# Performance work log

Measured on AMD Instinct MI355X. Metric: run time of the kernel, lower is better.

## Reference

```python
import jax, jax.numpy as jnp
import numpy as np

B, S, E = 32, 128, 128
NQ, NS = 100000, 512
QN, SN = 4, 10
S_MAX = 4
NEG = -1e30


def setup_inputs() -> dict:
    key = jax.random.key(0)
    ks = jax.random.split(key, 24)
    def nrm(k, shape, sc):
        return jax.random.normal(k, shape, jnp.float32) * sc
    inp = {}
    inp['question'] = jax.random.randint(ks[0], (B, S), 0, NQ, jnp.int32)
    inp['response'] = jax.random.randint(ks[1], (B, S), 0, 2, jnp.int32)
    inp['mask'] = jax.random.randint(ks[2], (B, S), 0, 2, jnp.int32)
    inp['q_neighbors'] = jax.random.randint(ks[3], (NQ, QN), 0, NS, jnp.int32)
    inp['s_neighbors'] = jax.random.randint(ks[4], (NS, SN), 0, NQ, jnp.int32)
    sidx = jax.random.randint(ks[5], (NQ, S_MAX), 0, NS, jnp.int32)
    inp['qs_table'] = jnp.zeros((NQ, NS), jnp.float32).at[jnp.arange(NQ)[:, None], sidx].set(1.0)
    inp['emb_q'] = nrm(ks[6], (NQ, E), 1.0)
    inp['emb_s'] = nrm(ks[7], (NS, E), 1.0)
    inp['emb_r'] = nrm(ks[8], (2, E), 1.0)
    s_in = 1.0 / np.sqrt(2 * E).astype(np.float32)
    s_e = 1.0 / np.sqrt(E).astype(np.float32)
    inp['W_ih'] = nrm(ks[9], (4 * E, 2 * E), s_in)
    inp['b_ih'] = nrm(ks[10], (4 * E,), s_in)
    inp['b_hh'] = nrm(ks[11], (4 * E,), s_in)
    inp['W_agg'] = nrm(ks[12], (3, E, E), s_e)
    inp['b_agg'] = nrm(ks[13], (3, E), s_e)
    inp['W_last'] = nrm(ks[14], (E, E), s_e)
    inp['b_last'] = nrm(ks[15], (E,), s_e)
    inp['W_query'] = nrm(ks[16], (E, E), s_e)
    inp['b_query'] = nrm(ks[17], (E,), s_e)
    inp['W_key'] = nrm(ks[18], (E, E), s_e)
    inp['b_key'] = nrm(ks[19], (E,), s_e)
    inp['w_W'] = nrm(ks[20], (2 * E,), s_in)
    inp['b_W'] = nrm(ks[21], (), s_in)
    return inp


def _forward(question, response, mask, q_neighbors, s_neighbors, qs_table,
             emb_q, emb_s, emb_r, W_ih, b_ih, b_hh, W_agg, b_agg, W_last, b_last,
             W_query, b_query, W_key, b_key, w_W, b_W):
    Bq, Sq = question.shape
    Ed = emb_q.shape[1]
    AGG = W_agg.shape[0]
    w_q, w_k = w_W[:Ed], w_W[Ed:]
    c_pad = jnp.tanh(b_query) @ w_k  # attention logit piece of an all-zero padded state
    pos = jnp.arange(Sq)

    def step(state_history, xs):
        t, q_t, r_t, m_t, q_next = xs
        # ---- multi-hop neighbor gather (q -> s -> q -> s) ----
        n1 = q_neighbors[q_t]              # [B,QN] skill ids
        n2 = s_neighbors[n1]               # [B,QN,SN] question ids
        n3 = q_neighbors[n2]               # [B,QN,SN,QN] skill ids
        e = [emb_q[q_t], emb_s[n1], emb_q[n2], emb_s[n3]]
        # triangular mean-aggregate (dropout is identity in eval mode)
        for i in range(AGG):
            for j in range(AGG - i):
                e[j] = jnp.tanh((e[j + 1].mean(-2) + e[j]) @ W_agg[j].T + b_agg[j])
        agg = jnp.tanh(e[0] @ W_last.T + b_last)
        emb_qt = jnp.where((m_t == 1)[:, None], agg, emb_q[q_t])
        # ---- LSTMCell with zero initial (h, c): W_hh @ 0 drops out, b_hh remains ----
        x = jnp.concatenate([emb_qt, emb_r[r_t]], -1)
        gates = x @ W_ih.T + b_ih + b_hh
        gi, gf, gg, go = jnp.split(gates, 4, -1)
        h = jax.nn.sigmoid(go) * jnp.tanh(jax.nn.sigmoid(gi) * jnp.tanh(gg))
        # ---- skills related to next question; zero-padded rows contribute exactly 0 ----
        vals, sidx = jax.lax.top_k(qs_table[q_next], S_MAX)
        emb_sk = emb_s[sidx] * (vals > 0.0)[..., None]
        qs_concat = jnp.concatenate([emb_q[q_next][:, None], emb_sk], 1)  # [B,1+S_MAX,E]
        # ---- hard recap: history steps whose question is a 2-hop neighbor of q_next ----
        q_rel = s_neighbors[q_neighbors[q_next]].reshape(Bq, -1)          # [B,QN*SN]
        matches = (question[:, :, None] == q_rel[:, None, :]).any(-1) & (pos[None, :] < t)
        n_sel = matches.sum(-1)
        P = (jnp.max(n_sel) - n_sel).astype(jnp.float32)  # zero-pad count to per-batch max
        # ---- predict: MLP_W(concat(Q,K)) is rank-1 => logit = a[b,q] + c[b,s] ----
        a = jnp.tanh(qs_concat @ W_key.T + b_key) @ w_q + b_W             # [B,Qd]
        c_hist = jnp.tanh(state_history @ W_query.T + b_query) @ w_k      # [B,S]
        c_cur = jnp.tanh(h @ W_query.T + b_query) @ w_k                   # [B]
        lh = jnp.where(matches[:, None, :], a[:, :, None] + c_hist[:, None, :], NEG)
        lc = a + c_cur[:, None]
        lp = a + c_pad
        m = jnp.maximum(jnp.maximum(lh.max(-1), lc), lp)
        Eh = jnp.exp(lh - m[:, :, None])
        Ec = jnp.exp(lc - m)
        Ep = jnp.exp(lp - m)
        g_hist = jnp.einsum('bqe,bse->bqs', qs_concat, state_history)
        g_cur = jnp.einsum('bqe,be->bq', qs_concat, h)
        denom = Eh.sum(-1) + Ec + P[:, None] * Ep  # zero-pad states counted analytically
        num = (Eh * g_hist).sum(-1) + Ec * g_cur   # pads multiply g=0 -> no numerator term
        y = jax.nn.sigmoid(jnp.sum(num / denom, axis=1))
        # original skips the state write at t == 0 (slot 0 stays zero forever)
        state_history = state_history.at[:, t].set(jnp.where(t > 0, h, jnp.zeros_like(h)))
        return state_history, y

    ts = jnp.arange(Sq - 1)
    xs = (ts, question[:, :-1].T, response[:, :-1].T, mask[:, :-1].T, question[:, 1:].T)
    init = jnp.zeros((Bq, Sq, Ed), jnp.float32)
    _, ys = jax.lax.scan(step, init, xs)
    return jnp.zeros((Bq, Sq), jnp.float32).at[:, 0].set(0.5).at[:, 1:].set(ys.T)


def reference(question, response, mask, q_neighbors, s_neighbors, qs_table,
              emb_q, emb_s, emb_r, W_ih, b_ih, b_hh, W_agg, b_agg, W_last, b_last,
              W_query, b_query, W_key, b_key, w_W, b_W):
    return _forward(question, response, mask, q_neighbors, s_neighbors, qs_table,
                    emb_q, emb_s, emb_r, W_ih, b_ih, b_hh, W_agg, b_agg, W_last, b_last,
                    W_query, b_query, W_key, b_key, w_W, b_W)
```

## Files before the change

kernel.cpp:

```cpp
#include <hip/hip_runtime.h>
#include <stdint.h>

#define NB 32
#define SEQ 128
#define EMB 128
#define NSTEP 127
#define NS 512

__device__ __forceinline__ float ftanh(float x){ float e=__expf(2.f*x); return 1.f-2.f/(e+1.f); }
__device__ __forceinline__ float fsig(float x){ return 1.f/(1.f+__expf(-x)); }
__device__ __forceinline__ float4 ld4(const float* p){ return *(const float4*)p; }

#define FMA_COL(acc, xv) \
  acc.x = fmaf(xv.x, w0.x, fmaf(xv.y, w1.x, fmaf(xv.z, w2.x, fmaf(xv.w, w3.x, acc.x)))); \
  acc.y = fmaf(xv.x, w0.y, fmaf(xv.y, w1.y, fmaf(xv.z, w2.y, fmaf(xv.w, w3.y, acc.y)))); \
  acc.z = fmaf(xv.x, w0.z, fmaf(xv.y, w1.z, fmaf(xv.z, w2.z, fmaf(xv.w, w3.z, acc.z)))); \
  acc.w = fmaf(xv.x, w0.w, fmaf(xv.y, w1.w, fmaf(xv.z, w2.w, fmaf(xv.w, w3.w, acc.w))));

template<int K, int XS>
__device__ __forceinline__ void gemm16(const float* __restrict__ WT, int NEtot,
                                       const float* __restrict__ Xl,
                                       const float* __restrict__ bias,
                                       float* __restrict__ outb )
{
  const int tid = threadIdx.x;
  const int et = tid & 31;
  const int rt = tid >> 5;
  const float* wp = WT + et*4;
  const float* x0 = Xl + (rt*2)*XS;
  const float* x1 = x0 + XS;
  float4 acc0 = {0.f,0.f,0.f,0.f}, acc1 = {0.f,0.f,0.f,0.f};
  float4 w0 = ld4(wp);
  float4 w1 = ld4(wp + NEtot);
  float4 w2 = ld4(wp + 2*NEtot);
  float4 w3 = ld4(wp + 3*NEtot);
  float4 xa = ld4(x0), xb = ld4(x1);
  #pragma unroll 8
  for (int k = 4; k < K; k += 4) {
    const float* wn = wp + (size_t)k*NEtot;
    float4 m0 = ld4(wn);
    float4 m1 = ld4(wn + NEtot);
    float4 m2 = ld4(wn + 2*NEtot);
    float4 m3 = ld4(wn + 3*NEtot);
    float4 ya = ld4(x0 + k), yb = ld4(x1 + k);
    FMA_COL(acc0, xa); FMA_COL(acc1, xb);
    w0=m0; w1=m1; w2=m2; w3=m3; xa=ya; xb=yb;
  }
  FMA_COL(acc0, xa); FMA_COL(acc1, xb);
  float4 bb = ld4(bias + et*4);
  acc0.x+=bb.x; acc0.y+=bb.y; acc0.z+=bb.z; acc0.w+=bb.w;
  acc1.x+=bb.x; acc1.y+=bb.y; acc1.z+=bb.z; acc1.w+=bb.w;
  *(float4*)(outb + (rt*2)*132 + et*4) = acc0;
  *(float4*)(outb + (rt*2+1)*132 + et*4) = acc1;
}
#undef FMA_COL

__global__ __launch_bounds__(256) void k_T(
    const float* __restrict__ W_agg, const float* __restrict__ W_last,
    const float* __restrict__ W_query, const float* __restrict__ W_ih,
    const float* __restrict__ b_ih, const float* __restrict__ b_hh,
    const float* __restrict__ b_query, const float* __restrict__ w_W,
    float* __restrict__ WT012, float* __restrict__ WLT, float* __restrict__ WQT,
    float* __restrict__ WIHT, float* __restrict__ BIH, float* __restrict__ CPAD)
{
  const int gid = blockIdx.x*256 + threadIdx.x;
  const int gsz = gridDim.x*256;
  for (int i = gid; i < 49152; i += gsz) {
    int j = i >> 14, rem = i & 16383, k = rem >> 7, e = rem & 127;
    WT012[i] = W_agg[j*16384 + e*128 + k];
  }
  for (int i = gid; i < 16384; i += gsz) {
    int k = i >> 7, e = i & 127;
    WLT[i] = W_last[e*128 + k];
    WQT[i] = W_query[e*128 + k];
  }
  for (int i = gid; i < 131072; i += gsz) {
    int k = i >> 9, e = i & 511;
    WIHT[i] = W_ih[e*256 + k];
  }
  for (int i = gid; i < 512; i += gsz) BIH[i] = b_ih[i] + b_hh[i];
  if (blockIdx.x == 0) {
    __shared__ float red[256];
    float v = (threadIdx.x < 128) ? ftanh(b_query[threadIdx.x]) * w_W[128 + threadIdx.x] : 0.f;
    red[threadIdx.x] = v; __syncthreads();
    #pragma unroll
    for (int s = 128; s > 0; s >>= 1) {
      if (threadIdx.x < s) red[threadIdx.x] += red[threadIdx.x + s];
      __syncthreads();
    }
    if (threadIdx.x == 0) CPAD[0] = red[0];
  }
}

__global__ __launch_bounds__(256) void k_pre(
    const int* __restrict__ s_neighbors, const int* __restrict__ q_neighbors,
    const float* __restrict__ emb_q, const float* __restrict__ emb_s,
    const float* __restrict__ WT012, const float* __restrict__ b_agg,
    float* __restrict__ E1, float* __restrict__ G1)
{
  __shared__ float XA[16*132];
  __shared__ float XB[16*132];
  __shared__ int idx[160];
  __shared__ int n3[64];
  const int tid = threadIdx.x;
  const int blk = blockIdx.x;
  if (blk < 32) {
    const int s0 = blk*16;
    if (tid < 160) idx[tid] = s_neighbors[s0*10 + tid];
    __syncthreads();
    for (int f = tid; f < 512; f += 256) {
      int r = f >> 5, e4 = (f & 31) << 2;
      float4 a = ld4(emb_s + (size_t)(s0+r)*128 + e4);
      float sx=0,sy=0,sz=0,sw=0;
      #pragma unroll
      for (int jj = 0; jj < 10; ++jj) {
        float4 q = ld4(emb_q + (size_t)idx[r*10+jj]*128 + e4);
        sx+=q.x; sy+=q.y; sz+=q.z; sw+=q.w;
      }
      float4 o; o.x=a.x+0.1f*sx; o.y=a.y+0.1f*sy; o.z=a.z+0.1f*sz; o.w=a.w+0.1f*sw;
      *(float4*)(XA + r*132 + e4) = o;
    }
    __syncthreads();
    gemm16<128,132>(WT012 + 16384, 128, XA, b_agg + 128, XB);
    __syncthreads();
    for (int f = tid; f < 2048; f += 256) {
      int r = f >> 7, e = f & 127;
      E1[(size_t)(s0+r)*128 + e] = ftanh(XB[r*132 + e]);
    }
  } else {
    const int p0 = (blk-32)*16;
    if (tid < 16) idx[tid] = s_neighbors[p0 + tid];
    __syncthreads();
    if (tid < 64) n3[tid] = q_neighbors[(size_t)idx[tid>>2]*4 + (tid&3)];
    __syncthreads();
    for (int f = tid; f < 512; f += 256) {
      int r = f >> 5, e4 = (f & 31) << 2;
      float4 a = ld4(emb_q + (size_t)idx[r]*128 + e4);
      float sx=0,sy=0,sz=0,sw=0;
      #pragma unroll
      for (int k = 0; k < 4; ++k) {
        float4 q = ld4(emb_s + (size_t)n3[r*4+k]*128 + e4);
        sx+=q.x; sy+=q.y; sz+=q.z; sw+=q.w;
      }
      float4 o; o.x=a.x+0.25f*sx; o.y=a.y+0.25f*sy; o.z=a.z+0.25f*sz; o.w=a.w+0.25f*sw;
      *(float4*)(XA + r*132 + e4) = o;
    }
    __syncthreads();
    gemm16<128,132>(WT012 + 32768, 128, XA, b_agg + 256, XB);
    __syncthreads();
    for (int f = tid; f < 2048; f += 256) {
      int r = f >> 7, e = f & 127;
      atomicAdd(&G1[(size_t)((p0+r)/10)*128 + e], ftanh(XB[r*132 + e]));
    }
  }
}

__global__ __launch_bounds__(256) void k_pre2(
    const float* __restrict__ E1, const float* __restrict__ G1,
    const float* __restrict__ WT012, const float* __restrict__ b_agg,
    float* __restrict__ E2)
{
  __shared__ float XA[16*132];
  __shared__ float XB[16*132];
  const int tid = threadIdx.x;
  const int s0 = blockIdx.x*16;
  for (int f = tid; f < 2048; f += 256) {
    int r = f >> 7, e = f & 127;
    XA[r*132 + e] = 0.1f*G1[(size_t)(s0+r)*128 + e] + E1[(size_t)(s0+r)*128 + e];
  }
  __syncthreads();
  gemm16<128,132>(WT012 + 16384, 128, XA, b_agg + 128, XB);
  __syncthreads();
  for (int f = tid; f < 2048; f += 256) {
    int r = f >> 7, e = f & 127;
    E2[(size_t)(s0+r)*128 + e] = ftanh(XB[r*132 + e]);
  }
}

__global__ __launch_bounds__(256) void k_chain(
    const int* __restrict__ question, const int* __restrict__ response,
    const int* __restrict__ maskp, const int* __restrict__ q_neighbors,
    const float* __restrict__ emb_q, const float* __restrict__ emb_s,
    const float* __restrict__ emb_r,
    const float* __restrict__ WT012, const float* __restrict__ WLT,
    const float* __restrict__ WQT, const float* __restrict__ WIHT,
    const float* __restrict__ BIH,
    const float* __restrict__ b_agg, const float* __restrict__ b_last,
    const float* __restrict__ b_query, const float* __restrict__ w_W,
    const float* __restrict__ E1, const float* __restrict__ E2,
    float* __restrict__ Hfull, float* __restrict__ Cq)
{
  __shared__ float P_[12688];
  __shared__ int qts[16], rts[16], mts[16], n1s[64];
  float* XA = P_;
  float* XB = P_ + 2112;
  float* M1 = P_ + 4224;
  float* M2 = P_ + 6272;
  float* G3 = P_ + 4224;
  float* XC = P_ + 8448;
  float* cq = P_ + 12672;

  const int tid = threadIdx.x;
  const int blk = blockIdx.x;

  if (tid < 16) {
    int rid = blk*16 + tid;
    int b = rid / 127, t = rid - b*127;
    qts[tid] = question[b*SEQ + t];
    rts[tid] = response[b*SEQ + t];
    mts[tid] = maskp[b*SEQ + t];
    cq[tid] = 0.f;
  }
  __syncthreads();
  if (tid < 64) n1s[tid] = q_neighbors[(size_t)qts[tid>>2]*4 + (tid&3)];
  __syncthreads();
  for (int f = tid; f < 512; f += 256) {
    int r = f >> 5, e4 = (f & 31) << 2;
    const int* nn = n1s + r*4;
    float4 a = ld4(emb_q + (size_t)qts[r]*128 + e4);
    float s1x=0,s1y=0,s1z=0,s1w=0, s2x=0,s2y=0,s2z=0,s2w=0, s3x=0,s3y=0,s3z=0,s3w=0;
    #pragma unroll
    for (int i = 0; i < 4; ++i) {
      float4 q1 = ld4(emb_s + (size_t)nn[i]*128 + e4);
      float4 q2 = ld4(E1 + (size_t)nn[i]*128 + e4);
      float4 q3 = ld4(E2 + (size_t)nn[i]*128 + e4);
      s1x+=q1.x; s1y+=q1.y; s1z+=q1.z; s1w+=q1.w;
      s2x+=q2.x; s2y+=q2.y; s2z+=q2.z; s2w+=q2.w;
      s3x+=q3.x; s3y+=q3.y; s3z+=q3.z; s3w+=q3.w;
    }
    float4 o; o.x=a.x+0.25f*s1x; o.y=a.y+0.25f*s1y; o.z=a.z+0.25f*s1z; o.w=a.w+0.25f*s1w;
    *(float4*)(XA + r*132 + e4) = o;
    float4 p; p.x=0.25f*s2x; p.y=0.25f*s2y; p.z=0.25f*s2z; p.w=0.25f*s2w;
    *(float4*)(M1 + r*128 + e4) = p;
    float4 u; u.x=0.25f*s3x; u.y=0.25f*s3y; u.z=0.25f*s3z; u.w=0.25f*s3w;
    *(float4*)(M2 + r*128 + e4) = u;
  }
  __syncthreads();
  gemm16<128,132>(WT012, 128, XA, b_agg, XB);
  __syncthreads();
  for (int f = tid; f < 2048; f += 256) {
    int r = f >> 7, e = f & 127;
    XB[r*132 + e] = M1[r*128 + e] + ftanh(XB[r*132 + e]);
  }
  __syncthreads();
  gemm16<128,132>(WT012, 128, XB, b_agg, XA);
  __syncthreads();
  for (int f = tid; f < 2048; f += 256) {
    int r = f >> 7, e = f & 127;
    XA[r*132 + e] = M2[r*128 + e] + ftanh(XA[r*132 + e]);
  }
  __syncthreads();
  gemm16<128,132>(WT012, 128, XA, b_agg, XB);
  __syncthreads();
  for (int f = tid; f < 2048; f += 256) {
    int r = f >> 7, e = f & 127;
    XB[r*132 + e] = ftanh(XB[r*132 + e]);
  }
  __syncthreads();
  gemm16<128,132>(WLT, 128, XB, b_last, XA);
  __syncthreads();
  for (int f = tid; f < 2048; f += 256) {
    int r = f >> 7, e = f & 127;
    float agg = ftanh(XA[r*132 + e]);
    XC[r*264 + e] = (mts[r] == 1) ? agg : emb_q[(size_t)qts[r]*128 + e];
    XC[r*264 + 128 + e] = emb_r[rts[r]*128 + e];
  }
  __syncthreads();
  gemm16<256,264>(WIHT,       512, XC, BIH,       XA);
  gemm16<256,264>(WIHT + 256, 512, XC, BIH + 256, XB);
  gemm16<256,264>(WIHT + 384, 512, XC, BIH + 384, G3);
  __syncthreads();
  for (int f = tid; f < 2048; f += 256) {
    int r = f >> 7, e = f & 127;
    float gi = XA[r*132 + e], gg = XB[r*132 + e], go = G3[r*132 + e];
    float h = fsig(go) * ftanh(fsig(gi) * ftanh(gg));
    XC[r*264 + e] = h;
    Hfull[(size_t)(blk*16 + r)*128 + e] = h;
  }
  __syncthreads();
  gemm16<128,264>(WQT, 128, XC, b_query, XA);
  __syncthreads();
  {
    const int et = tid & 31, rt = tid >> 5;
    const float* wk = w_W + 128 + et*4;
    float4 wv = ld4(wk);
    #pragma unroll
    for (int rr = 0; rr < 2; ++rr) {
      int r = rt*2 + rr;
      const float* o = XA + r*132 + et*4;
      float s = ftanh(o[0])*wv.x + ftanh(o[1])*wv.y + ftanh(o[2])*wv.z + ftanh(o[3])*wv.w;
      atomicAdd(&cq[r], s);
    }
  }
  __syncthreads();
  if (tid < 16) Cq[blk*16 + tid] = cq[tid];
}

__global__ __launch_bounds__(128) void k_match_t(
    const int* __restrict__ question, const int* __restrict__ q_neighbors,
    const int* __restrict__ s_neighbors,
    int* __restrict__ nsel, unsigned long long* __restrict__ mwords,
    float* __restrict__ Pmax)
{
  __shared__ int nq[4];
  __shared__ int qr[40];
  __shared__ unsigned long long wv[2];
  const int tid = threadIdx.x;
  const int t = blockIdx.x;
  int pm = 0;
  for (int b = 0; b < NB; ++b) {
    const int q_next = question[b*SEQ + t + 1];
    if (tid < 4) nq[tid] = q_neighbors[(size_t)q_next*4 + tid];
    __syncthreads();
    if (tid < 40) qr[tid] = s_neighbors[(size_t)nq[tid/10]*10 + tid%10];
    __syncthreads();
    bool pred = false;
    if (tid < t) {
      int qp = question[b*SEQ + tid];
      #pragma unroll 8
      for (int i = 0; i < 40; ++i) pred |= (qp == qr[i]);
    }
    unsigned long long bal = __ballot(pred);
    if ((tid & 63) == 0) wv[tid >> 6] = bal;
    __syncthreads();
    if (tid == 0) {
      mwords[((size_t)b*NSTEP + t)*2 + 0] = wv[0];
      mwords[((size_t)b*NSTEP + t)*2 + 1] = wv[1];
      int ns = __popcll(wv[0]) + __popcll(wv[1]);
      nsel[b*NSTEP + t] = ns;
      pm = max(pm, ns);
    }
    __syncthreads();
  }
  if (tid == 0) Pmax[t] = (float)pm;
}

__device__ __forceinline__ float bsum128(float v, float* red) {
  const int tid = threadIdx.x;
  __syncthreads();
  red[tid] = v;
  __syncthreads();
  #pragma unroll
  for (int s = 64; s > 0; s >>= 1) {
    if (tid < s) red[tid] += red[tid + s];
    __syncthreads();
  }
  return red[0];
}
__device__ __forceinline__ float bmax128(float v, float* red) {
  const int tid = threadIdx.x;
  __syncthreads();
  red[tid] = v;
  __syncthreads();
  #pragma unroll
  for (int s = 64; s > 0; s >>= 1) {
    if (tid < s) red[tid] = fmaxf(red[tid], red[tid + s]);
    __syncthreads();
  }
  return red[0];
}

__global__ __launch_bounds__(128) void k_attn(
    const int* __restrict__ question, const float* __restrict__ qs_table,
    const float* __restrict__ emb_q, const float* __restrict__ emb_s,
    const float* __restrict__ CPAD,
    const float* __restrict__ Hfull, const float* __restrict__ Cq,
    const int* __restrict__ nsel, const unsigned long long* __restrict__ mwords,
    const float* __restrict__ Pmax, float* __restrict__ out)
{
  __shared__ float red[128];
  __shared__ float us[128];
  __shared__ int cols[8];
  __shared__ int cnt;
  const int tid = threadIdx.x;
  const int bid = blockIdx.x;
  const int b = bid / NSTEP, t = bid % NSTEP;
  const size_t bt = (size_t)b*NSTEP + t;
  const int q_next = question[b*SEQ + t + 1];

  if (tid == 0) cnt = 0;
  __syncthreads();
  #pragma unroll
  for (int m = 0; m < 4; ++m) {
    int c = tid + 128*m;
    float v = qs_table[(size_t)q_next*NS + c];
    if (v > 0.f) {
      int p = atomicAdd(&cnt, 1);
      if (p < 8) cols[p] = c;
    }
  }
  __syncthreads();
  const int nc = min(cnt, 4);
  {
    float ue = emb_q[(size_t)q_next*EMB + tid];
    for (int i = 0; i < nc; ++i) ue += emb_s[(size_t)cols[i]*EMB + tid];
    us[tid] = ue;
  }
  const float c_pad = CPAD[0];
  const float P = Pmax[t] - (float)nsel[bt];

  const unsigned long long w0 = mwords[bt*2 + 0];
  const unsigned long long w1 = mwords[bt*2 + 1];
  const bool matched = (tid < 64) ? ((w0 >> tid) & 1ull)
                                  : ((w1 >> (tid - 64)) & 1ull);
  const float c_cur = Cq[bt];
  float Cp = 0.f;
  if (matched) Cp = (tid == 0) ? c_pad : Cq[(size_t)b*NSTEP + tid];
  float Mh = bmax128(matched ? Cp : -3.0e38f, red);
  float M = fmaxf(fmaxf(Mh, c_cur), c_pad);
  float wgt = matched ? __expf(Cp - M) : 0.f;
  float Sexp = bsum128(wgt, red);
  float dotp = 0.f;
  if (matched && tid >= 1) {
    const float* hp = Hfull + ((size_t)b*NSTEP + tid)*EMB;
    float s = 0.f;
    for (int e = 0; e < 128; e += 4) {
      float4 h4 = ld4(hp + e);
      s = fmaf(us[e],h4.x, fmaf(us[e+1],h4.y, fmaf(us[e+2],h4.z, fmaf(us[e+3],h4.w, s))));
    }
    dotp = s;
  }
  float Snum = bsum128(wgt * dotp, red);
  float gc = bsum128(us[tid] * Hfull[bt*EMB + tid], red);
  float Ec = __expf(c_cur - M), Ep = __expf(c_pad - M);
  float D = Sexp + Ec + P * Ep;
  float numt = Snum + Ec * gc;
  if (tid == 0) {
    out[b*SEQ + t + 1] = fsig(numt / D);
    if (t == 0) out[b*SEQ] = 0.5f;
  }
}

extern "C" void kernel_launch(void* const* d_in, const int* in_sizes, int n_in,
                              void* d_out, int out_size, void* d_ws, size_t ws_size,
                              hipStream_t stream) {
  const int* question    = (const int*)d_in[0];
  const int* response    = (const int*)d_in[1];
  const int* maskp       = (const int*)d_in[2];
  const int* q_neighbors = (const int*)d_in[3];
  const int* s_neighbors = (const int*)d_in[4];
  const float* qs_table  = (const float*)d_in[5];
  const float* emb_q     = (const float*)d_in[6];
  const float* emb_s     = (const float*)d_in[7];
  const float* emb_r     = (const float*)d_in[8];
  const float* W_ih      = (const float*)d_in[9];
  const float* b_ih      = (const float*)d_in[10];
  const float* b_hh      = (const float*)d_in[11];
  const float* W_agg     = (const float*)d_in[12];
  const float* b_agg     = (const float*)d_in[13];
  const float* W_last    = (const float*)d_in[14];
  const float* b_last    = (const float*)d_in[15];
  const float* W_query   = (const float*)d_in[16];
  const float* b_query   = (const float*)d_in[17];
  const float* w_W       = (const float*)d_in[20];
  float* out = (float*)d_out;

  float* ws = (float*)d_ws;
  float* WT012 = ws;
  float* WLT   = ws + 49152;
  float* WQT   = ws + 65536;
  float* WIHT  = ws + 81920;
  float* BIH   = ws + 212992;
  float* CPAD  = ws + 213504;
  float* E1    = ws + 213520;
  float* G1    = ws + 279056;
  float* E2    = ws + 344592;
  float* Hfull = ws + 410128;
  float* Cq    = ws + 930320;
  float* Pmax  = ws + 934384;
  int*   nselp = (int*)(ws + 934512);
  unsigned long long* mwords =
      (unsigned long long*)(((uintptr_t)(ws + 938576) + 15) & ~(uintptr_t)15);

  hipMemsetAsync(G1, 0, 65536*sizeof(float), stream);
  k_T<<<dim3(64), dim3(256), 0, stream>>>(
      W_agg, W_last, W_query, W_ih, b_ih, b_hh, b_query, w_W,
      WT012, WLT, WQT, WIHT, BIH, CPAD);
  k_pre<<<dim3(352), dim3(256), 0, stream>>>(
      s_neighbors, q_neighbors, emb_q, emb_s, WT012, b_agg, E1, G1);
  k_pre2<<<dim3(32), dim3(256), 0, stream>>>(E1, G1, WT012, b_agg, E2);
  k_chain<<<dim3(254), dim3(256), 0, stream>>>(
      question, response, maskp, q_neighbors, emb_q, emb_s, emb_r,
      WT012, WLT, WQT, WIHT, BIH, b_agg, b_last, b_query, w_W,
      E1, E2, Hfull, Cq);
  k_match_t<<<dim3(NSTEP), dim3(128), 0, stream>>>(
      question, q_neighbors, s_neighbors, nselp, mwords, Pmax);
  k_attn<<<dim3(NB*NSTEP), dim3(128), 0, stream>>>(
      question, qs_table, emb_q, emb_s, CPAD, Hfull, Cq,
      nselp, mwords, Pmax, out);
}
```

Measured before the change: 441.2 us.

## Halve GEMM row tiles to double grid size, use wave-shuffle reductions

```diff
diff --git a/kernel.cpp b/kernel.cpp
--- a/kernel.cpp
+++ b/kernel.cpp
@@ -18,40 +18,39 @@
   acc.w = fmaf(xv.x, w0.w, fmaf(xv.y, w1.w, fmaf(xv.z, w2.w, fmaf(xv.w, w3.w, acc.w))));
 
 template<int K, int XS>
-__device__ __forceinline__ void gemm16(const float* __restrict__ WT, int NEtot,
-                                       const float* __restrict__ Xl,
-                                       const float* __restrict__ bias,
-                                       float* __restrict__ outb )
+__device__ __forceinline__ void gemm8(const float* __restrict__ WT, int NEtot,
+                                      const float* __restrict__ Xl,
+                                      const float* __restrict__ bias,
+                                      float* __restrict__ outb )
 {
   const int tid = threadIdx.x;
   const int et = tid & 31;
   const int rt = tid >> 5;
   const float* wp = WT + et*4;
-  const float* x0 = Xl + (rt*2)*XS;
-  const float* x1 = x0 + XS;
-  float4 acc0 = {0.f,0.f,0.f,0.f}, acc1 = {0.f,0.f,0.f,0.f};
-  float4 w0 = ld4(wp);
-  float4 w1 = ld4(wp + NEtot);
-  float4 w2 = ld4(wp + 2*NEtot);
-  float4 w3 = ld4(wp + 3*NEtot);
-  float4 xa = ld4(x0), xb = ld4(x1);
-  #pragma unroll 8
-  for (int k = 4; k < K; k += 4) {
-    const float* wn = wp + (size_t)k*NEtot;
-    float4 m0 = ld4(wn);
-    float4 m1 = ld4(wn + NEtot);
-    float4 m2 = ld4(wn + 2*NEtot);
-    float4 m3 = ld4(wn + 3*NEtot);
-    float4 ya = ld4(x0 + k), yb = ld4(x1 + k);
-    FMA_COL(acc0, xa); FMA_COL(acc1, xb);
-    w0=m0; w1=m1; w2=m2; w3=m3; xa=ya; xb=yb;
-  }
-  FMA_COL(acc0, xa); FMA_COL(acc1, xb);
+  const float* xr = Xl + rt*XS;
+  constexpr int G = K/4;
+  float4 wb[4][4];
+  #pragma unroll
+  for (int p = 0; p < 3; ++p) {
+    const float* w = wp + (size_t)(4*p)*NEtot;
+    wb[p][0]=ld4(w); wb[p][1]=ld4(w+NEtot);
+    wb[p][2]=ld4(w+2*NEtot); wb[p][3]=ld4(w+3*NEtot);
+  }
+  float4 acc = {0.f,0.f,0.f,0.f};
+  #pragma unroll
+  for (int g = 0; g < G; ++g) {
+    float4 w0=wb[g&3][0], w1=wb[g&3][1], w2=wb[g&3][2], w3=wb[g&3][3];
+    if (g+3 < G) {
+      const float* w = wp + (size_t)(4*(g+3))*NEtot;
+      wb[(g+3)&3][0]=ld4(w); wb[(g+3)&3][1]=ld4(w+NEtot);
+      wb[(g+3)&3][2]=ld4(w+2*NEtot); wb[(g+3)&3][3]=ld4(w+3*NEtot);
+    }
+    float4 xa = ld4(xr + 4*g);
+    FMA_COL(acc, xa);
+  }
   float4 bb = ld4(bias + et*4);
-  acc0.x+=bb.x; acc0.y+=bb.y; acc0.z+=bb.z; acc0.w+=bb.w;
-  acc1.x+=bb.x; acc1.y+=bb.y; acc1.z+=bb.z; acc1.w+=bb.w;
-  *(float4*)(outb + (rt*2)*132 + et*4) = acc0;
-  *(float4*)(outb + (rt*2+1)*132 + et*4) = acc1;
+  acc.x+=bb.x; acc.y+=bb.y; acc.z+=bb.z; acc.w+=bb.w;
+  *(float4*)(outb + rt*132 + et*4) = acc;
 }
 #undef FMA_COL
 
@@ -61,7 +60,8 @@
     const float* __restrict__ b_ih, const float* __restrict__ b_hh,
     const float* __restrict__ b_query, const float* __restrict__ w_W,
     float* __restrict__ WT012, float* __restrict__ WLT, float* __restrict__ WQT,
-    float* __restrict__ WIHT, float* __restrict__ BIH, float* __restrict__ CPAD)
+    float* __restrict__ WIHT, float* __restrict__ BIH, float* __restrict__ CPAD,
+    float* __restrict__ G1, int* __restrict__ Pmaxi)
 {
   const int gid = blockIdx.x*256 + threadIdx.x;
   const int gsz = gridDim.x*256;
@@ -78,7 +78,9 @@
     int k = i >> 9, e = i & 511;
     WIHT[i] = W_ih[e*256 + k];
   }
+  for (int i = gid; i < 65536; i += gsz) G1[i] = 0.f;
   for (int i = gid; i < 512; i += gsz) BIH[i] = b_ih[i] + b_hh[i];
+  for (int i = gid; i < 128; i += gsz) Pmaxi[i] = 0;
   if (blockIdx.x == 0) {
     __shared__ float red[256];
     float v = (threadIdx.x < 128) ? ftanh(b_query[threadIdx.x]) * w_W[128 + threadIdx.x] : 0.f;
@@ -98,18 +100,18 @@
     const float* __restrict__ WT012, const float* __restrict__ b_agg,
     float* __restrict__ E1, float* __restrict__ G1)
 {
-  __shared__ float XA[16*132];
-  __shared__ float XB[16*132];
-  __shared__ int idx[160];
-  __shared__ int n3[64];
+  __shared__ float XA[8*132];
+  __shared__ float XB[8*132];
+  __shared__ int idx[80];
+  __shared__ int n3[32];
   const int tid = threadIdx.x;
   const int blk = blockIdx.x;
-  if (blk < 32) {
-    const int s0 = blk*16;
-    if (tid < 160) idx[tid] = s_neighbors[s0*10 + tid];
-    __syncthreads();
-    for (int f = tid; f < 512; f += 256) {
-      int r = f >> 5, e4 = (f & 31) << 2;
+  if (blk < 64) {
+    const int s0 = blk*8;
+    if (tid < 80) idx[tid] = s_neighbors[s0*10 + tid];
+    __syncthreads();
+    {
+      int r = tid >> 5, e4 = (tid & 31) << 2;
       float4 a = ld4(emb_s + (size_t)(s0+r)*128 + e4);
       float sx=0,sy=0,sz=0,sw=0;
       #pragma unroll
@@ -121,20 +123,20 @@
       *(float4*)(XA + r*132 + e4) = o;
     }
     __syncthreads();
-    gemm16<128,132>(WT012 + 16384, 128, XA, b_agg + 128, XB);
-    __syncthreads();
-    for (int f = tid; f < 2048; f += 256) {
+    gemm8<128,132>(WT012 + 16384, 128, XA, b_agg + 128, XB);
+    __syncthreads();
+    for (int f = tid; f < 1024; f += 256) {
       int r = f >> 7, e = f & 127;
       E1[(size_t)(s0+r)*128 + e] = ftanh(XB[r*132 + e]);
     }
   } else {
-    const int p0 = (blk-32)*16;
-    if (tid < 16) idx[tid] = s_neighbors[p0 + tid];
-    __syncthreads();
-    if (tid < 64) n3[tid] = q_neighbors[(size_t)idx[tid>>2]*4 + (tid&3)];
-    __syncthreads();
-    for (int f = tid; f < 512; f += 256) {
-      int r = f >> 5, e4 = (f & 31) << 2;
+    const int p0 = (blk-64)*8;
+    if (tid < 8) idx[tid] = s_neighbors[p0 + tid];
+    __syncthreads();
+    if (tid < 32) n3[tid] = q_neighbors[(size_t)idx[tid>>2]*4 + (tid&3)];
+    __syncthreads();
+    {
+      int r = tid >> 5, e4 = (tid & 31) << 2;
       float4 a = ld4(emb_q + (size_t)idx[r]*128 + e4);
       float sx=0,sy=0,sz=0,sw=0;
       #pragma unroll
@@ -146,9 +148,9 @@
       *(float4*)(XA + r*132 + e4) = o;
     }
     __syncthreads();
-    gemm16<128,132>(WT012 + 32768, 128, XA, b_agg + 256, XB);
-    __syncthreads();
-    for (int f = tid; f < 2048; f += 256) {
+    gemm8<128,132>(WT012 + 32768, 128, XA, b_agg + 256, XB);
+    __syncthreads();
+    for (int f = tid; f < 1024; f += 256) {
       int r = f >> 7, e = f & 127;
       atomicAdd(&G1[(size_t)((p0+r)/10)*128 + e], ftanh(XB[r*132 + e]));
     }
@@ -160,18 +162,18 @@
     const float* __restrict__ WT012, const float* __restrict__ b_agg,
     float* __restrict__ E2)
 {
-  __shared__ float XA[16*132];
-  __shared__ float XB[16*132];
-  const int tid = threadIdx.x;
-  const int s0 = blockIdx.x*16;
-  for (int f = tid; f < 2048; f += 256) {
+  __shared__ float XA[8*132];
+  __shared__ float XB[8*132];
+  const int tid = threadIdx.x;
+  const int s0 = blockIdx.x*8;
+  for (int f = tid; f < 1024; f += 256) {
     int r = f >> 7, e = f & 127;
     XA[r*132 + e] = 0.1f*G1[(size_t)(s0+r)*128 + e] + E1[(size_t)(s0+r)*128 + e];
   }
   __syncthreads();
-  gemm16<128,132>(WT012 + 16384, 128, XA, b_agg + 128, XB);
-  __syncthreads();
-  for (int f = tid; f < 2048; f += 256) {
+  gemm8<128,132>(WT012 + 16384, 128, XA, b_agg + 128, XB);
+  __syncthreads();
+  for (int f = tid; f < 1024; f += 256) {
     int r = f >> 7, e = f & 127;
     E2[(size_t)(s0+r)*128 + e] = ftanh(XB[r*132 + e]);
   }
@@ -190,32 +192,28 @@
     const float* __restrict__ E1, const float* __restrict__ E2,
     float* __restrict__ Hfull, float* __restrict__ Cq)
 {
-  __shared__ float P_[12688];
-  __shared__ int qts[16], rts[16], mts[16], n1s[64];
-  float* XA = P_;
-  float* XB = P_ + 2112;
-  float* M1 = P_ + 4224;
-  float* M2 = P_ + 6272;
-  float* G3 = P_ + 4224;
-  float* XC = P_ + 8448;
-  float* cq = P_ + 12672;
+  __shared__ float XA[8*132];
+  __shared__ float XB[8*132];
+  __shared__ float M1[8*132];
+  __shared__ float M2[8*132];
+  __shared__ float XC[8*264];
+  __shared__ int qts[8], rts[8], mts[8], n1s[32];
 
   const int tid = threadIdx.x;
   const int blk = blockIdx.x;
 
-  if (tid < 16) {
-    int rid = blk*16 + tid;
+  if (tid < 8) {
+    int rid = blk*8 + tid;
     int b = rid / 127, t = rid - b*127;
     qts[tid] = question[b*SEQ + t];
     rts[tid] = response[b*SEQ + t];
     mts[tid] = maskp[b*SEQ + t];
-    cq[tid] = 0.f;
-  }
-  __syncthreads();
-  if (tid < 64) n1s[tid] = q_neighbors[(size_t)qts[tid>>2]*4 + (tid&3)];
-  __syncthreads();
-  for (int f = tid; f < 512; f += 256) {
-    int r = f >> 5, e4 = (f & 31) << 2;
+  }
+  __syncthreads();
+  if (tid < 32) n1s[tid] = q_neighbors[(size_t)qts[tid>>2]*4 + (tid&3)];
+  __syncthreads();
+  {
+    int r = tid >> 5, e4 = (tid & 31) << 2;
     const int* nn = n1s + r*4;
     float4 a = ld4(emb_q + (size_t)qts[r]*128 + e4);
     float s1x=0,s1y=0,s1z=0,s1w=0, s2x=0,s2y=0,s2z=0,s2w=0, s3x=0,s3y=0,s3z=0,s3w=0;
@@ -231,84 +229,70 @@
     float4 o; o.x=a.x+0.25f*s1x; o.y=a.y+0.25f*s1y; o.z=a.z+0.25f*s1z; o.w=a.w+0.25f*s1w;
     *(float4*)(XA + r*132 + e4) = o;
     float4 p; p.x=0.25f*s2x; p.y=0.25f*s2y; p.z=0.25f*s2z; p.w=0.25f*s2w;
-    *(float4*)(M1 + r*128 + e4) = p;
+    *(float4*)(M1 + r*132 + e4) = p;
     float4 u; u.x=0.25f*s3x; u.y=0.25f*s3y; u.z=0.25f*s3z; u.w=0.25f*s3w;
-    *(float4*)(M2 + r*128 + e4) = u;
-  }
-  __syncthreads();
-  gemm16<128,132>(WT012, 128, XA, b_agg, XB);
-  __syncthreads();
-  for (int f = tid; f < 2048; f += 256) {
-    int r = f >> 7, e = f & 127;
-    XB[r*132 + e] = M1[r*128 + e] + ftanh(XB[r*132 + e]);
-  }
-  __syncthreads();
-  gemm16<128,132>(WT012, 128, XB, b_agg, XA);
-  __syncthreads();
-  for (int f = tid; f < 2048; f += 256) {
-    int r = f >> 7, e = f & 127;
-    XA[r*132 + e] = M2[r*128 + e] + ftanh(XA[r*132 + e]);
-  }
-  __syncthreads();
-  gemm16<128,132>(WT012, 128, XA, b_agg, XB);
-  __syncthreads();
-  for (int f = tid; f < 2048; f += 256) {
-    int r = f >> 7, e = f & 127;
-    XB[r*132 + e] = ftanh(XB[r*132 + e]);
-  }
-  __syncthreads();
-  gemm16<128,132>(WLT, 128, XB, b_last, XA);
-  __syncthreads();
-  for (int f = tid; f < 2048; f += 256) {
+    *(float4*)(M2 + r*132 + e4) = u;
+  }
+  __syncthreads();
+  gemm8<128,132>(WT012, 128, XA, b_agg, XB);
+  __syncthreads();
+  for (int f = tid; f < 1056; f += 256) XB[f] = M1[f] + ftanh(XB[f]);
+  __syncthreads();
+  gemm8<128,132>(WT012, 128, XB, b_agg, XA);
+  __syncthreads();
+  for (int f = tid; f < 1056; f += 256) XA[f] = M2[f] + ftanh(XA[f]);
+  __syncthreads();
+  gemm8<128,132>(WT012, 128, XA, b_agg, XB);
+  __syncthreads();
+  for (int f = tid; f < 1056; f += 256) XB[f] = ftanh(XB[f]);
+  __syncthreads();
+  gemm8<128,132>(WLT, 128, XB, b_last, XA);
+  __syncthreads();
+  for (int f = tid; f < 1024; f += 256) {
     int r = f >> 7, e = f & 127;
     float agg = ftanh(XA[r*132 + e]);
     XC[r*264 + e] = (mts[r] == 1) ? agg : emb_q[(size_t)qts[r]*128 + e];
     XC[r*264 + 128 + e] = emb_r[rts[r]*128 + e];
   }
   __syncthreads();
-  gemm16<256,264>(WIHT,       512, XC, BIH,       XA);
-  gemm16<256,264>(WIHT + 256, 512, XC, BIH + 256, XB);
-  gemm16<256,264>(WIHT + 384, 512, XC, BIH + 384, G3);
-  __syncthreads();
-  for (int f = tid; f < 2048; f += 256) {
+  gemm8<256,264>(WIHT,       512, XC, BIH,       XA);
+  gemm8<256,264>(WIHT + 256, 512, XC, BIH + 256, XB);
+  gemm8<256,264>(WIHT + 384, 512, XC, BIH + 384, M1);
+  __syncthreads();
+  for (int f = tid; f < 1024; f += 256) {
     int r = f >> 7, e = f & 127;
-    float gi = XA[r*132 + e], gg = XB[r*132 + e], go = G3[r*132 + e];
+    float gi = XA[r*132 + e], gg = XB[r*132 + e], go = M1[r*132 + e];
     float h = fsig(go) * ftanh(fsig(gi) * ftanh(gg));
     XC[r*264 + e] = h;
-    Hfull[(size_t)(blk*16 + r)*128 + e] = h;
-  }
-  __syncthreads();
-  gemm16<128,264>(WQT, 128, XC, b_query, XA);
+    Hfull[(size_t)(blk*8 + r)*128 + e] = h;
+  }
+  __syncthreads();
+  gemm8<128,264>(WQT, 128, XC, b_query, XA);
   __syncthreads();
   {
     const int et = tid & 31, rt = tid >> 5;
-    const float* wk = w_W + 128 + et*4;
-    float4 wv = ld4(wk);
+    float4 o = ld4(XA + rt*132 + et*4);
+    float4 wv = ld4(w_W + 128 + et*4);
+    float s = ftanh(o.x)*wv.x + ftanh(o.y)*wv.y + ftanh(o.z)*wv.z + ftanh(o.w)*wv.w;
     #pragma unroll
-    for (int rr = 0; rr < 2; ++rr) {
-      int r = rt*2 + rr;
-      const float* o = XA + r*132 + et*4;
-      float s = ftanh(o[0])*wv.x + ftanh(o[1])*wv.y + ftanh(o[2])*wv.z + ftanh(o[3])*wv.w;
-      atomicAdd(&cq[r], s);
-    }
-  }
-  __syncthreads();
-  if (tid < 16) Cq[blk*16 + tid] = cq[tid];
-}
-
-__global__ __launch_bounds__(128) void k_match_t(
+    for (int off = 16; off > 0; off >>= 1) s += __shfl_down(s, off);
+    if (et == 0) Cq[blk*8 + rt] = s;
+  }
+}
+
+__global__ __launch_bounds__(128) void k_match(
     const int* __restrict__ question, const int* __restrict__ q_neighbors,
     const int* __restrict__ s_neighbors,
     int* __restrict__ nsel, unsigned long long* __restrict__ mwords,
-    float* __restrict__ Pmax)
+    int* __restrict__ Pmaxi)
 {
   __shared__ int nq[4];
   __shared__ int qr[40];
   __shared__ unsigned long long wv[2];
   const int tid = threadIdx.x;
   const int t = blockIdx.x;
-  int pm = 0;
-  for (int b = 0; b < NB; ++b) {
+  for (int bb = 0; bb < 8; ++bb) {
+    const int b = blockIdx.y*8 + bb;
     const int q_next = question[b*SEQ + t + 1];
     if (tid < 4) nq[tid] = q_neighbors[(size_t)q_next*4 + tid];
     __syncthreads();
@@ -328,36 +312,21 @@
       mwords[((size_t)b*NSTEP + t)*2 + 1] = wv[1];
       int ns = __popcll(wv[0]) + __popcll(wv[1]);
       nsel[b*NSTEP + t] = ns;
-      pm = max(pm, ns);
-    }
-    __syncthreads();
-  }
-  if (tid == 0) Pmax[t] = (float)pm;
-}
-
-__device__ __forceinline__ float bsum128(float v, float* red) {
-  const int tid = threadIdx.x;
-  __syncthreads();
-  red[tid] = v;
-  __syncthreads();
+      atomicMax(&Pmaxi[t], ns);
+    }
+    __syncthreads();
+  }
+}
+
+__device__ __forceinline__ float wredsum(float v) {
   #pragma unroll
-  for (int s = 64; s > 0; s >>= 1) {
-    if (tid < s) red[tid] += red[tid + s];
-    __syncthreads();
-  }
-  return red[0];
-}
-__device__ __forceinline__ float bmax128(float v, float* red) {
-  const int tid = threadIdx.x;
-  __syncthreads();
-  red[tid] = v;
-  __syncthreads();
+  for (int o = 32; o > 0; o >>= 1) v += __shfl_down(v, o);
+  return v;
+}
+__device__ __forceinline__ float wredmax(float v) {
   #pragma unroll
-  for (int s = 64; s > 0; s >>= 1) {
-    if (tid < s) red[tid] = fmaxf(red[tid], red[tid + s]);
-    __syncthreads();
-  }
-  return red[0];
+  for (int o = 32; o > 0; o >>= 1) v = fmaxf(v, __shfl_down(v, o));
+  return v;
 }
 
 __global__ __launch_bounds__(128) void k_attn(
@@ -366,13 +335,15 @@
     const float* __restrict__ CPAD,
     const float* __restrict__ Hfull, const float* __restrict__ Cq,
     const int* __restrict__ nsel, const unsigned long long* __restrict__ mwords,
-    const float* __restrict__ Pmax, float* __restrict__ out)
-{
-  __shared__ float red[128];
+    const int* __restrict__ Pmaxi, float* __restrict__ out)
+{
   __shared__ float us[128];
   __shared__ int cols[8];
   __shared__ int cnt;
-  const int tid = threadIdx.x;
+  __shared__ float smx[2];
+  __shared__ float s3[2][3];
+  const int tid = threadIdx.x;
+  const int wid = tid >> 6;
   const int bid = blockIdx.x;
   const int b = bid / NSTEP, t = bid % NSTEP;
   const size_t bt = (size_t)b*NSTEP + t;
@@ -397,35 +368,43 @@
     us[tid] = ue;
   }
   const float c_pad = CPAD[0];
-  const float P = Pmax[t] - (float)nsel[bt];
+  const float P = (float)(Pmaxi[t] - nsel[bt]);
 
   const unsigned long long w0 = mwords[bt*2 + 0];
   const unsigned long long w1 = mwords[bt*2 + 1];
   const bool matched = (tid < 64) ? ((w0 >> tid) & 1ull)
                                   : ((w1 >> (tid - 64)) & 1ull);
   const float c_cur = Cq[bt];
-  float Cp = 0.f;
-  if (matched) Cp = (tid == 0) ? c_pad : Cq[(size_t)b*NSTEP + tid];
-  float Mh = bmax128(matched ? Cp : -3.0e38f, red);
-  float M = fmaxf(fmaxf(Mh, c_cur), c_pad);
+  float Cp = matched ? ((tid == 0) ? c_pad : Cq[(size_t)b*NSTEP + tid]) : -3.0e38f;
+  float mh = wredmax(Cp);
+  if ((tid & 63) == 0) smx[wid] = mh;
+  __syncthreads();
+  float M = fmaxf(fmaxf(smx[0], smx[1]), fmaxf(c_cur, c_pad));
   float wgt = matched ? __expf(Cp - M) : 0.f;
-  float Sexp = bsum128(wgt, red);
   float dotp = 0.f;
   if (matched && tid >= 1) {
     const float* hp = Hfull + ((size_t)b*NSTEP + tid)*EMB;
     float s = 0.f;
+    #pragma unroll 8
     for (int e = 0; e < 128; e += 4) {
       float4 h4 = ld4(hp + e);
       s = fmaf(us[e],h4.x, fmaf(us[e+1],h4.y, fmaf(us[e+2],h4.z, fmaf(us[e+3],h4.w, s))));
     }
     dotp = s;
   }
-  float Snum = bsum128(wgt * dotp, red);
-  float gc = bsum128(us[tid] * Hfull[bt*EMB + tid], red);
-  float Ec = __expf(c_cur - M), Ep = __expf(c_pad - M);
-  float D = Sexp + Ec + P * Ep;
-  float numt = Snum + Ec * gc;
+  float gcp = us[tid] * Hfull[bt*EMB + tid];
+  float a0 = wredsum(wgt);
+  float a1 = wredsum(wgt * dotp);
+  float a2 = wredsum(gcp);
+  if ((tid & 63) == 0) { s3[wid][0] = a0; s3[wid][1] = a1; s3[wid][2] = a2; }
+  __syncthreads();
   if (tid == 0) {
+    float Sexp = s3[0][0] + s3[1][0];
+    float Snum = s3[0][1] + s3[1][1];
+    float gc   = s3[0][2] + s3[1][2];
+    float Ec = __expf(c_cur - M), Ep = __expf(c_pad - M);
+    float D = Sexp + Ec + P * Ep;
+    float numt = Snum + Ec * gc;
     out[b*SEQ + t + 1] = fsig(numt / D);
     if (t == 0) out[b*SEQ] = 0.5f;
   }
@@ -467,25 +446,24 @@
   float* E2    = ws + 344592;
   float* Hfull = ws + 410128;
   float* Cq    = ws + 930320;
-  float* Pmax  = ws + 934384;
+  int*   Pmaxi = (int*)(ws + 934384);
   int*   nselp = (int*)(ws + 934512);
   unsigned long long* mwords =
       (unsigned long long*)(((uintptr_t)(ws + 938576) + 15) & ~(uintptr_t)15);
 
-  hipMemsetAsync(G1, 0, 65536*sizeof(float), stream);
   k_T<<<dim3(64), dim3(256), 0, stream>>>(
       W_agg, W_last, W_query, W_ih, b_ih, b_hh, b_query, w_W,
-      WT012, WLT, WQT, WIHT, BIH, CPAD);
-  k_pre<<<dim3(352), dim3(256), 0, stream>>>(
+      WT012, WLT, WQT, WIHT, BIH, CPAD, G1, Pmaxi);
+  k_pre<<<dim3(704), dim3(256), 0, stream>>>(
       s_neighbors, q_neighbors, emb_q, emb_s, WT012, b_agg, E1, G1);
-  k_pre2<<<dim3(32), dim3(256), 0, stream>>>(E1, G1, WT012, b_agg, E2);
-  k_chain<<<dim3(254), dim3(256), 0, stream>>>(
+  k_pre2<<<dim3(64), dim3(256), 0, stream>>>(E1, G1, WT012, b_agg, E2);
+  k_chain<<<dim3(508), dim3(256), 0, stream>>>(
       question, response, maskp, q_neighbors, emb_q, emb_s, emb_r,
       WT012, WLT, WQT, WIHT, BIH, b_agg, b_last, b_query, w_W,
       E1, E2, Hfull, Cq);
-  k_match_t<<<dim3(NSTEP), dim3(128), 0, stream>>>(
-      question, q_neighbors, s_neighbors, nselp, mwords, Pmax);
+  k_match<<<dim3(NSTEP, 4), dim3(128), 0, stream>>>(
+      question, q_neighbors, s_neighbors, nselp, mwords, Pmaxi);
   k_attn<<<dim3(NB*NSTEP), dim3(128), 0, stream>>>(
       question, qs_table, emb_q, emb_s, CPAD, Hfull, Cq,
-      nselp, mwords, Pmax, out);
-}
+      nselp, mwords, Pmaxi, out);
+}
```

New measurement: 778.3 us. +76.4%, slower.
